# Optimization experiments

Measured on AMD Instinct MI355X. Metric: run time of the kernel, lower is better.

The kernel has to match this reference:

```python
import jax, jax.numpy as jnp
import numpy as np

H = 50  # hidden_size

def setup_inputs() -> dict:
    key = jax.random.key(0)
    ks = jax.random.split(key, 7)
    B, T, I = 8192, 2048, 1
    s_ih = 1.0 / np.sqrt(H)
    x = jax.random.normal(ks[0], (B, T, I), dtype=jnp.float32)
    # PyTorch nn.LSTM params, gate order (i, f, g, o)
    W_ih = jax.random.uniform(ks[1], (4 * H, I), minval=-s_ih, maxval=s_ih, dtype=jnp.float32)
    W_hh = jax.random.uniform(ks[2], (4 * H, H), minval=-s_ih, maxval=s_ih, dtype=jnp.float32)
    b_ih = jax.random.uniform(ks[3], (4 * H,), minval=-s_ih, maxval=s_ih, dtype=jnp.float32)
    b_hh = jax.random.uniform(ks[4], (4 * H,), minval=-s_ih, maxval=s_ih, dtype=jnp.float32)
    W_lin = jax.random.uniform(ks[5], (1, H), minval=-s_ih, maxval=s_ih, dtype=jnp.float32)
    b_lin = jax.random.uniform(ks[6], (1,), minval=-s_ih, maxval=s_ih, dtype=jnp.float32)
    return {"x": x, "W_ih": W_ih, "W_hh": W_hh, "b_ih": b_ih, "b_hh": b_hh,
            "W_lin": W_lin, "b_lin": b_lin}

def _lstm_last_h(x, W_ih, W_hh, b_ih, b_hh):
    B = x.shape[0]
    # precompute input contribution per timestep: [T, B, 4H]
    xg = jnp.einsum('bti,gi->tbg', x, W_ih) + (b_ih + b_hh)  # [T,B,4H]

    def step(carry, xg_t):
        h, c = carry
        z = xg_t + h @ W_hh.T  # [B,4H]
        i = jax.nn.sigmoid(z[:, :H])
        f = jax.nn.sigmoid(z[:, H:2 * H])
        g = jnp.tanh(z[:, 2 * H:3 * H])
        o = jax.nn.sigmoid(z[:, 3 * H:])
        c = f * c + i * g
        h = o * jnp.tanh(c)
        return (h, c), None

    h0 = jnp.zeros((B, H), dtype=x.dtype)
    c0 = jnp.zeros((B, H), dtype=x.dtype)
    (h_last, _), _ = jax.lax.scan(step, (h0, c0), xg)
    return h_last  # [B,H]

def reference(x, W_ih, W_hh, b_ih, b_hh, W_lin, b_lin):
    h_last = _lstm_last_h(x, W_ih, W_hh, b_ih, b_hh)
    return h_last @ W_lin.T + b_lin  # [B,1]
```

## Files before the change

kernel.cpp:

```cpp
#include <hip/hip_runtime.h>


#define HID   50
#define NSTEP 2048
#define BPB   16
#define HSTR  72

typedef _Float16 half8   __attribute__((ext_vector_type(8)));
typedef float    float4v __attribute__((ext_vector_type(4)));
typedef float    float2v __attribute__((ext_vector_type(2)));

__device__ __forceinline__ float2v lo2(float4v v) { float2v r; r[0] = v[0]; r[1] = v[1]; return r; }
__device__ __forceinline__ float2v hi2(float4v v) { float2v r; r[0] = v[2]; r[1] = v[3]; return r; }

__device__ __forceinline__ float2v exp2v(float2v x) {
    float2v r;
    r[0] = __builtin_amdgcn_exp2f(x[0]);
    r[1] = __builtin_amdgcn_exp2f(x[1]);
    return r;
}

__device__ __forceinline__ float2v gate_pairs2(float2v zi, float2v zf, float2v zg,
                                               float2v zo, float2v& c) {
    float2v ei = exp2v(zi);
    float2v ef = exp2v(zf);
    float2v Eg = exp2v(zg);
    float2v eo = exp2v(zo);
    float2v t1  = (1.0f + ei) * (1.0f + Eg);
    float2v pf  = 1.0f + ef;
    float2v num = c * t1 + pf * (Eg - 1.0f);
    float2v D   = t1 * pf;
    float   rP  = __builtin_amdgcn_rcpf(D[0] * D[1]);
    float2v Dsw; Dsw[0] = D[1]; Dsw[1] = D[0];
    c = num * Dsw * rP;
    float2v a = 2.8853900817779268f * c;
    a[0] = fminf(fmaxf(a[0], -24.0f), 24.0f);
    a[1] = fminf(fmaxf(a[1], -24.0f), 24.0f);
    float2v Ec  = exp2v(a);
    float2v den = (1.0f + eo) * (1.0f + Ec);
    float   rQ  = __builtin_amdgcn_rcpf(den[0] * den[1]);
    float2v dsw; dsw[0] = den[1]; dsw[1] = den[0];
    return (Ec - 1.0f) * dsw * rQ;
}

__global__ __launch_bounds__(256, 2) void lstm_fused(
    const float* __restrict__ x,
    const float* __restrict__ W_ih,
    const float* __restrict__ W_hh,
    const float* __restrict__ b_ih,
    const float* __restrict__ b_hh,
    const float* __restrict__ W_lin,
    const float* __restrict__ b_lin,
    float* __restrict__ out)
{
    __shared__ __align__(16) _Float16 hbuf[2][BPB][HSTR];

    const int tid  = threadIdx.x;
    const int wave = tid >> 6;
    const int lane = tid & 63;
    const int col  = lane & 15;
    const int quad = lane >> 4;
    const int b0   = blockIdx.x * BPB;
    const int j    = wave * 16 + col;

    for (int i = tid; i < 2 * BPB * HSTR; i += 256)
        (&hbuf[0][0][0])[i] = (_Float16)0.0f;
    __syncthreads();
    if (tid < BPB) {
        hbuf[0][tid][HID]     = (_Float16)x[(size_t)(b0 + tid) * NSTEP];
        hbuf[0][tid][HID + 1] = (_Float16)1.0f;
        hbuf[1][tid][HID + 1] = (_Float16)1.0f;
    }

    const float LOG2E = 1.4426950408889634f;
    half8 bfrag[4][2];
    for (int g = 0; g < 4; ++g) {
        const float sc = (g == 2) ? (2.0f * LOG2E) : (-LOG2E);
        for (int kt = 0; kt < 2; ++kt) {
            half8 f;
            #pragma unroll
            for (int jj = 0; jj < 8; ++jj) {
                int k = kt * 32 + quad * 8 + jj;
                float v = 0.0f;
                if (j < HID) {
                    int row = g * HID + j;
                    if (k < HID)           v = W_hh[row * HID + k];
                    else if (k == HID)     v = W_ih[row];
                    else if (k == HID + 1) v = b_ih[row] + b_hh[row];
                }
                f[jj] = (_Float16)(v * sc);
            }
            bfrag[g][kt] = f;
        }
    }

    float2v c01 = {0.f, 0.f};
    float2v c23 = {0.f, 0.f};
    const bool xloader = (wave == 3) && (quad == 0);
    const float* xrow = x + (size_t)(b0 + col) * NSTEP;
    const float4v Z4 = {0.f, 0.f, 0.f, 0.f};

    __syncthreads();

    if (blockIdx.x & 1) {
        __builtin_amdgcn_s_sleep(15);
    }

#define STEP(CUR, NXT, T)                                                        \
    {                                                                            \
        float xn = 0.f;                                                          \
        if (xloader) {                                                           \
            int tt = ((T) + 1 < NSTEP) ? ((T) + 1) : (NSTEP - 1);                \
            xn = xrow[tt];                                                       \
        }                                                                        \
        const _Float16* arow = &hbuf[CUR][col][0];                               \
        half8 a0 = *(const half8*)(arow + quad * 8);                             \
        half8 a1 = *(const half8*)(arow + 32 + quad * 8);                        \
        float4v d0, d1, d2, d3;                                                  \
        d0 = __builtin_amdgcn_mfma_f32_16x16x32_f16(a0, bfrag[0][0], Z4, 0, 0, 0); \
        d1 = __builtin_amdgcn_mfma_f32_16x16x32_f16(a0, bfrag[1][0], Z4, 0, 0, 0); \
        d2 = __builtin_amdgcn_mfma_f32_16x16x32_f16(a0, bfrag[2][0], Z4, 0, 0, 0); \
        d3 = __builtin_amdgcn_mfma_f32_16x16x32_f16(a0, bfrag[3][0], Z4, 0, 0, 0); \
        d0 = __builtin_amdgcn_mfma_f32_16x16x32_f16(a1, bfrag[0][1], d0, 0, 0, 0); \
        d1 = __builtin_amdgcn_mfma_f32_16x16x32_f16(a1, bfrag[1][1], d1, 0, 0, 0); \
        d2 = __builtin_amdgcn_mfma_f32_16x16x32_f16(a1, bfrag[2][1], d2, 0, 0, 0); \
        d3 = __builtin_amdgcn_mfma_f32_16x16x32_f16(a1, bfrag[3][1], d3, 0, 0, 0); \
        float2v h01 = gate_pairs2(lo2(d0), lo2(d1), lo2(d2), lo2(d3), c01);      \
        if (j < HID) {                                                           \
            hbuf[NXT][quad * 4 + 0][j] = (_Float16)h01[0];                       \
            hbuf[NXT][quad * 4 + 1][j] = (_Float16)h01[1];                       \
        }                                                                        \
        float2v h23 = gate_pairs2(hi2(d0), hi2(d1), hi2(d2), hi2(d3), c23);      \
        if (j < HID) {                                                           \
            hbuf[NXT][quad * 4 + 2][j] = (_Float16)h23[0];                       \
            hbuf[NXT][quad * 4 + 3][j] = (_Float16)h23[1];                       \
        }                                                                        \
        if (xloader)                                                             \
            hbuf[NXT][col][HID] = (_Float16)xn;                                  \
        __syncthreads();                                                         \
    }

    for (int t = 0; t < NSTEP; t += 2) {
        STEP(0, 1, t)
        STEP(1, 0, t + 1)
    }
#undef STEP

    if (tid < BPB) {
        float s = b_lin[0];
        for (int k = 0; k < HID; ++k)
            s += (float)hbuf[0][tid][k] * W_lin[k];
        out[b0 + tid] = s;
    }
}

extern "C" void kernel_launch(void* const* d_in, const int* in_sizes, int n_in,
                              void* d_out, int out_size, void* d_ws, size_t ws_size,
                              hipStream_t stream) {
    const float* x     = (const float*)d_in[0];
    const float* W_ih  = (const float*)d_in[1];
    const float* W_hh  = (const float*)d_in[2];
    const float* b_ih  = (const float*)d_in[3];
    const float* b_hh  = (const float*)d_in[4];
    const float* W_lin = (const float*)d_in[5];
    const float* b_lin = (const float*)d_in[6];
    float* outp = (float*)d_out;
    dim3 grid(8192 / BPB), block(256);
    hipLaunchKernelGGL(lstm_fused, grid, block, 0, stream,
                       x, W_ih, W_hh, b_ih, b_hh, W_lin, b_lin, outp);
}
```

Baseline: 1.338 ms.

## Process two 16-row batch tiles per block to interleave independent recurrences

```diff
diff --git a/kernel.cpp b/kernel.cpp
--- a/kernel.cpp
+++ b/kernel.cpp
@@ -3,7 +3,7 @@
 
 #define HID   50
 #define NSTEP 2048
-#define BPB   16
+#define BPB   32
 #define HSTR  72
 
 typedef _Float16 half8   __attribute__((ext_vector_type(8)));
@@ -43,7 +43,7 @@
     return (Ec - 1.0f) * dsw * rQ;
 }
 
-__global__ __launch_bounds__(256, 2) void lstm_fused(
+__global__ __launch_bounds__(256, 1) void lstm_fused(
     const float* __restrict__ x,
     const float* __restrict__ W_ih,
     const float* __restrict__ W_hh,
@@ -53,7 +53,7 @@
     const float* __restrict__ b_lin,
     float* __restrict__ out)
 {
-    __shared__ __align__(16) _Float16 hbuf[2][BPB][HSTR];
+    __shared__ __align__(16) _Float16 hbuf[2][2][16][HSTR];
 
     const int tid  = threadIdx.x;
     const int wave = tid >> 6;
@@ -63,13 +63,14 @@
     const int b0   = blockIdx.x * BPB;
     const int j    = wave * 16 + col;
 
-    for (int i = tid; i < 2 * BPB * HSTR; i += 256)
-        (&hbuf[0][0][0])[i] = (_Float16)0.0f;
+    for (int i = tid; i < 2 * 2 * 16 * HSTR; i += 256)
+        (&hbuf[0][0][0][0])[i] = (_Float16)0.0f;
     __syncthreads();
     if (tid < BPB) {
-        hbuf[0][tid][HID]     = (_Float16)x[(size_t)(b0 + tid) * NSTEP];
-        hbuf[0][tid][HID + 1] = (_Float16)1.0f;
-        hbuf[1][tid][HID + 1] = (_Float16)1.0f;
+        int g = tid >> 4, r = tid & 15;
+        hbuf[0][g][r][HID]     = (_Float16)x[(size_t)(b0 + tid) * NSTEP];
+        hbuf[0][g][r][HID + 1] = (_Float16)1.0f;
+        hbuf[1][g][r][HID + 1] = (_Float16)1.0f;
     }
 
     const float LOG2E = 1.4426950408889634f;
@@ -94,50 +95,62 @@
         }
     }
 
-    float2v c01 = {0.f, 0.f};
-    float2v c23 = {0.f, 0.f};
-    const bool xloader = (wave == 3) && (quad == 0);
-    const float* xrow = x + (size_t)(b0 + col) * NSTEP;
+    float2v cA01 = {0.f, 0.f}, cA23 = {0.f, 0.f};
+    float2v cB01 = {0.f, 0.f}, cB23 = {0.f, 0.f};
+
+    const bool xloader = (wave == 3) && (quad < 2);
+    const float* xrow = x + (size_t)(b0 + quad * 16 + col) * NSTEP;
     const float4v Z4 = {0.f, 0.f, 0.f, 0.f};
 
     __syncthreads();
 
-    if (blockIdx.x & 1) {
-        __builtin_amdgcn_s_sleep(15);
-    }
-
-#define STEP(CUR, NXT, T)                                                        \
-    {                                                                            \
-        float xn = 0.f;                                                          \
-        if (xloader) {                                                           \
-            int tt = ((T) + 1 < NSTEP) ? ((T) + 1) : (NSTEP - 1);                \
-            xn = xrow[tt];                                                       \
-        }                                                                        \
-        const _Float16* arow = &hbuf[CUR][col][0];                               \
-        half8 a0 = *(const half8*)(arow + quad * 8);                             \
-        half8 a1 = *(const half8*)(arow + 32 + quad * 8);                        \
-        float4v d0, d1, d2, d3;                                                  \
-        d0 = __builtin_amdgcn_mfma_f32_16x16x32_f16(a0, bfrag[0][0], Z4, 0, 0, 0); \
-        d1 = __builtin_amdgcn_mfma_f32_16x16x32_f16(a0, bfrag[1][0], Z4, 0, 0, 0); \
-        d2 = __builtin_amdgcn_mfma_f32_16x16x32_f16(a0, bfrag[2][0], Z4, 0, 0, 0); \
-        d3 = __builtin_amdgcn_mfma_f32_16x16x32_f16(a0, bfrag[3][0], Z4, 0, 0, 0); \
-        d0 = __builtin_amdgcn_mfma_f32_16x16x32_f16(a1, bfrag[0][1], d0, 0, 0, 0); \
-        d1 = __builtin_amdgcn_mfma_f32_16x16x32_f16(a1, bfrag[1][1], d1, 0, 0, 0); \
-        d2 = __builtin_amdgcn_mfma_f32_16x16x32_f16(a1, bfrag[2][1], d2, 0, 0, 0); \
-        d3 = __builtin_amdgcn_mfma_f32_16x16x32_f16(a1, bfrag[3][1], d3, 0, 0, 0); \
-        float2v h01 = gate_pairs2(lo2(d0), lo2(d1), lo2(d2), lo2(d3), c01);      \
-        if (j < HID) {                                                           \
-            hbuf[NXT][quad * 4 + 0][j] = (_Float16)h01[0];                       \
-            hbuf[NXT][quad * 4 + 1][j] = (_Float16)h01[1];                       \
-        }                                                                        \
-        float2v h23 = gate_pairs2(hi2(d0), hi2(d1), hi2(d2), hi2(d3), c23);      \
-        if (j < HID) {                                                           \
-            hbuf[NXT][quad * 4 + 2][j] = (_Float16)h23[0];                       \
-            hbuf[NXT][quad * 4 + 3][j] = (_Float16)h23[1];                       \
-        }                                                                        \
-        if (xloader)                                                             \
-            hbuf[NXT][col][HID] = (_Float16)xn;                                  \
-        __syncthreads();                                                         \
+#define STEP(CUR, NXT, T)                                                          \
+    {                                                                              \
+        float xn = 0.f;                                                            \
+        if (xloader) {                                                             \
+            int tt = ((T) + 1 < NSTEP) ? ((T) + 1) : (NSTEP - 1);                  \
+            xn = xrow[tt];                                                         \
+        }                                                                          \
+        const _Float16* arowA = &hbuf[CUR][0][col][0];                             \
+        const _Float16* arowB = &hbuf[CUR][1][col][0];                             \
+        half8 A0 = *(const half8*)(arowA + quad * 8);                              \
+        half8 A1 = *(const half8*)(arowA + 32 + quad * 8);                         \
+        half8 B0 = *(const half8*)(arowB + quad * 8);                              \
+        half8 B1 = *(const half8*)(arowB + 32 + quad * 8);                         \
+        float4v dA0, dA1, dA2, dA3, dB0, dB1, dB2, dB3;                            \
+        dA0 = __builtin_amdgcn_mfma_f32_16x16x32_f16(A0, bfrag[0][0], Z4, 0, 0, 0); \
+        dA1 = __builtin_amdgcn_mfma_f32_16x16x32_f16(A0, bfrag[1][0], Z4, 0, 0, 0); \
+        dA2 = __builtin_amdgcn_mfma_f32_16x16x32_f16(A0, bfrag[2][0], Z4, 0, 0, 0); \
+        dA3 = __builtin_amdgcn_mfma_f32_16x16x32_f16(A0, bfrag[3][0], Z4, 0, 0, 0); \
+        dB0 = __builtin_amdgcn_mfma_f32_16x16x32_f16(B0, bfrag[0][0], Z4, 0, 0, 0); \
+        dB1 = __builtin_amdgcn_mfma_f32_16x16x32_f16(B0, bfrag[1][0], Z4, 0, 0, 0); \
+        dB2 = __builtin_amdgcn_mfma_f32_16x16x32_f16(B0, bfrag[2][0], Z4, 0, 0, 0); \
+        dB3 = __builtin_amdgcn_mfma_f32_16x16x32_f16(B0, bfrag[3][0], Z4, 0, 0, 0); \
+        dA0 = __builtin_amdgcn_mfma_f32_16x16x32_f16(A1, bfrag[0][1], dA0, 0, 0, 0); \
+        dA1 = __builtin_amdgcn_mfma_f32_16x16x32_f16(A1, bfrag[1][1], dA1, 0, 0, 0); \
+        dA2 = __builtin_amdgcn_mfma_f32_16x16x32_f16(A1, bfrag[2][1], dA2, 0, 0, 0); \
+        dA3 = __builtin_amdgcn_mfma_f32_16x16x32_f16(A1, bfrag[3][1], dA3, 0, 0, 0); \
+        dB0 = __builtin_amdgcn_mfma_f32_16x16x32_f16(B1, bfrag[0][1], dB0, 0, 0, 0); \
+        dB1 = __builtin_amdgcn_mfma_f32_16x16x32_f16(B1, bfrag[1][1], dB1, 0, 0, 0); \
+        dB2 = __builtin_amdgcn_mfma_f32_16x16x32_f16(B1, bfrag[2][1], dB2, 0, 0, 0); \
+        dB3 = __builtin_amdgcn_mfma_f32_16x16x32_f16(B1, bfrag[3][1], dB3, 0, 0, 0); \
+        float2v hA01 = gate_pairs2(lo2(dA0), lo2(dA1), lo2(dA2), lo2(dA3), cA01);  \
+        float2v hB01 = gate_pairs2(lo2(dB0), lo2(dB1), lo2(dB2), lo2(dB3), cB01);  \
+        float2v hA23 = gate_pairs2(hi2(dA0), hi2(dA1), hi2(dA2), hi2(dA3), cA23);  \
+        float2v hB23 = gate_pairs2(hi2(dB0), hi2(dB1), hi2(dB2), hi2(dB3), cB23);  \
+        if (j < HID) {                                                             \
+            hbuf[NXT][0][quad * 4 + 0][j] = (_Float16)hA01[0];                     \
+            hbuf[NXT][0][quad * 4 + 1][j] = (_Float16)hA01[1];                     \
+            hbuf[NXT][0][quad * 4 + 2][j] = (_Float16)hA23[0];                     \
+            hbuf[NXT][0][quad * 4 + 3][j] = (_Float16)hA23[1];                     \
+            hbuf[NXT][1][quad * 4 + 0][j] = (_Float16)hB01[0];                     \
+            hbuf[NXT][1][quad * 4 + 1][j] = (_Float16)hB01[1];                     \
+            hbuf[NXT][1][quad * 4 + 2][j] = (_Float16)hB23[0];                     \
+            hbuf[NXT][1][quad * 4 + 3][j] = (_Float16)hB23[1];                     \
+        }                                                                          \
+        if (xloader)                                                               \
+            hbuf[NXT][quad][col][HID] = (_Float16)xn;                              \
+        __syncthreads();                                                           \
     }
 
     for (int t = 0; t < NSTEP; t += 2) {
@@ -147,9 +160,10 @@
 #undef STEP
 
     if (tid < BPB) {
+        int g = tid >> 4, r = tid & 15;
         float s = b_lin[0];
         for (int k = 0; k < HID; ++k)
-            s += (float)hbuf[0][tid][k] * W_lin[k];
+            s += (float)hbuf[0][g][r][k] * W_lin[k];
         out[b0 + tid] = s;
     }
 }
```

New measurement: 1.543 ms. 15.4% more time.

## Interleave two 16-sequence groups per block to overlap MFMA with gate math

Applied to the files above, without the earlier changes.

```diff
diff --git a/kernel.cpp b/kernel.cpp
--- a/kernel.cpp
+++ b/kernel.cpp
@@ -3,7 +3,7 @@
 
 #define HID   50
 #define NSTEP 2048
-#define BPB   16
+#define BPB   32
 #define HSTR  72
 
 typedef _Float16 half8   __attribute__((ext_vector_type(8)));
@@ -43,7 +43,7 @@
     return (Ec - 1.0f) * dsw * rQ;
 }
 
-__global__ __launch_bounds__(256, 2) void lstm_fused(
+__global__ __launch_bounds__(256, 1) void lstm_fused(
     const float* __restrict__ x,
     const float* __restrict__ W_ih,
     const float* __restrict__ W_hh,
@@ -53,7 +53,7 @@
     const float* __restrict__ b_lin,
     float* __restrict__ out)
 {
-    __shared__ __align__(16) _Float16 hbuf[2][BPB][HSTR];
+    __shared__ __align__(16) _Float16 hbuf[2][16][HSTR];
 
     const int tid  = threadIdx.x;
     const int wave = tid >> 6;
@@ -63,13 +63,13 @@
     const int b0   = blockIdx.x * BPB;
     const int j    = wave * 16 + col;
 
-    for (int i = tid; i < 2 * BPB * HSTR; i += 256)
+    for (int i = tid; i < 2 * 16 * HSTR; i += 256)
         (&hbuf[0][0][0])[i] = (_Float16)0.0f;
     __syncthreads();
     if (tid < BPB) {
-        hbuf[0][tid][HID]     = (_Float16)x[(size_t)(b0 + tid) * NSTEP];
-        hbuf[0][tid][HID + 1] = (_Float16)1.0f;
-        hbuf[1][tid][HID + 1] = (_Float16)1.0f;
+        int g = tid >> 4, r = tid & 15;
+        hbuf[g][r][HID]     = (_Float16)x[(size_t)(b0 + tid) * NSTEP];
+        hbuf[g][r][HID + 1] = (_Float16)1.0f;
     }
 
     const float LOG2E = 1.4426950408889634f;
@@ -94,62 +94,99 @@
         }
     }
 
-    float2v c01 = {0.f, 0.f};
-    float2v c23 = {0.f, 0.f};
+    float2v cA01 = {0.f, 0.f}, cA23 = {0.f, 0.f};
+    float2v cB01 = {0.f, 0.f}, cB23 = {0.f, 0.f};
+
     const bool xloader = (wave == 3) && (quad == 0);
-    const float* xrow = x + (size_t)(b0 + col) * NSTEP;
+    const float* xrowA = x + (size_t)(b0 + col) * NSTEP;
+    const float* xrowB = x + (size_t)(b0 + 16 + col) * NSTEP;
     const float4v Z4 = {0.f, 0.f, 0.f, 0.f};
 
     __syncthreads();
 
-    if (blockIdx.x & 1) {
-        __builtin_amdgcn_s_sleep(15);
-    }
-
-#define STEP(CUR, NXT, T)                                                        \
-    {                                                                            \
-        float xn = 0.f;                                                          \
-        if (xloader) {                                                           \
-            int tt = ((T) + 1 < NSTEP) ? ((T) + 1) : (NSTEP - 1);                \
-            xn = xrow[tt];                                                       \
-        }                                                                        \
-        const _Float16* arow = &hbuf[CUR][col][0];                               \
-        half8 a0 = *(const half8*)(arow + quad * 8);                             \
-        half8 a1 = *(const half8*)(arow + 32 + quad * 8);                        \
-        float4v d0, d1, d2, d3;                                                  \
-        d0 = __builtin_amdgcn_mfma_f32_16x16x32_f16(a0, bfrag[0][0], Z4, 0, 0, 0); \
-        d1 = __builtin_amdgcn_mfma_f32_16x16x32_f16(a0, bfrag[1][0], Z4, 0, 0, 0); \
-        d2 = __builtin_amdgcn_mfma_f32_16x16x32_f16(a0, bfrag[2][0], Z4, 0, 0, 0); \
-        d3 = __builtin_amdgcn_mfma_f32_16x16x32_f16(a0, bfrag[3][0], Z4, 0, 0, 0); \
-        d0 = __builtin_amdgcn_mfma_f32_16x16x32_f16(a1, bfrag[0][1], d0, 0, 0, 0); \
-        d1 = __builtin_amdgcn_mfma_f32_16x16x32_f16(a1, bfrag[1][1], d1, 0, 0, 0); \
-        d2 = __builtin_amdgcn_mfma_f32_16x16x32_f16(a1, bfrag[2][1], d2, 0, 0, 0); \
-        d3 = __builtin_amdgcn_mfma_f32_16x16x32_f16(a1, bfrag[3][1], d3, 0, 0, 0); \
-        float2v h01 = gate_pairs2(lo2(d0), lo2(d1), lo2(d2), lo2(d3), c01);      \
-        if (j < HID) {                                                           \
-            hbuf[NXT][quad * 4 + 0][j] = (_Float16)h01[0];                       \
-            hbuf[NXT][quad * 4 + 1][j] = (_Float16)h01[1];                       \
-        }                                                                        \
-        float2v h23 = gate_pairs2(hi2(d0), hi2(d1), hi2(d2), hi2(d3), c23);      \
-        if (j < HID) {                                                           \
-            hbuf[NXT][quad * 4 + 2][j] = (_Float16)h23[0];                       \
-            hbuf[NXT][quad * 4 + 3][j] = (_Float16)h23[1];                       \
-        }                                                                        \
-        if (xloader)                                                             \
-            hbuf[NXT][col][HID] = (_Float16)xn;                                  \
-        __syncthreads();                                                         \
-    }
-
-    for (int t = 0; t < NSTEP; t += 2) {
-        STEP(0, 1, t)
-        STEP(1, 0, t + 1)
-    }
-#undef STEP
+    float4v zA0, zA1, zA2, zA3, zB0, zB1, zB2, zB3;
+
+    {
+        const _Float16* ar = &hbuf[1][col][0];
+        half8 a0 = *(const half8*)(ar + quad * 8);
+        half8 a1 = *(const half8*)(ar + 32 + quad * 8);
+        zB0 = __builtin_amdgcn_mfma_f32_16x16x32_f16(a0, bfrag[0][0], Z4, 0, 0, 0);
+        zB1 = __builtin_amdgcn_mfma_f32_16x16x32_f16(a0, bfrag[1][0], Z4, 0, 0, 0);
+        zB2 = __builtin_amdgcn_mfma_f32_16x16x32_f16(a0, bfrag[2][0], Z4, 0, 0, 0);
+        zB3 = __builtin_amdgcn_mfma_f32_16x16x32_f16(a0, bfrag[3][0], Z4, 0, 0, 0);
+        zB0 = __builtin_amdgcn_mfma_f32_16x16x32_f16(a1, bfrag[0][1], zB0, 0, 0, 0);
+        zB1 = __builtin_amdgcn_mfma_f32_16x16x32_f16(a1, bfrag[1][1], zB1, 0, 0, 0);
+        zB2 = __builtin_amdgcn_mfma_f32_16x16x32_f16(a1, bfrag[2][1], zB2, 0, 0, 0);
+        zB3 = __builtin_amdgcn_mfma_f32_16x16x32_f16(a1, bfrag[3][1], zB3, 0, 0, 0);
+    }
+    __syncthreads();
+
+    for (int t = 0; t < NSTEP; ++t) {
+        {
+            float xn = 0.f;
+            if (xloader) {
+                int tt = (t + 1 < NSTEP) ? (t + 1) : (NSTEP - 1);
+                xn = xrowB[tt];
+            }
+            const _Float16* ar = &hbuf[0][col][0];
+            half8 a0 = *(const half8*)(ar + quad * 8);
+            half8 a1 = *(const half8*)(ar + 32 + quad * 8);
+            float2v h01 = gate_pairs2(lo2(zB0), lo2(zB1), lo2(zB2), lo2(zB3), cB01);
+            float2v h23 = gate_pairs2(hi2(zB0), hi2(zB1), hi2(zB2), hi2(zB3), cB23);
+            zA0 = __builtin_amdgcn_mfma_f32_16x16x32_f16(a0, bfrag[0][0], Z4, 0, 0, 0);
+            zA1 = __builtin_amdgcn_mfma_f32_16x16x32_f16(a0, bfrag[1][0], Z4, 0, 0, 0);
+            zA2 = __builtin_amdgcn_mfma_f32_16x16x32_f16(a0, bfrag[2][0], Z4, 0, 0, 0);
+            zA3 = __builtin_amdgcn_mfma_f32_16x16x32_f16(a0, bfrag[3][0], Z4, 0, 0, 0);
+            zA0 = __builtin_amdgcn_mfma_f32_16x16x32_f16(a1, bfrag[0][1], zA0, 0, 0, 0);
+            zA1 = __builtin_amdgcn_mfma_f32_16x16x32_f16(a1, bfrag[1][1], zA1, 0, 0, 0);
+            zA2 = __builtin_amdgcn_mfma_f32_16x16x32_f16(a1, bfrag[2][1], zA2, 0, 0, 0);
+            zA3 = __builtin_amdgcn_mfma_f32_16x16x32_f16(a1, bfrag[3][1], zA3, 0, 0, 0);
+            if (j < HID) {
+                hbuf[1][quad * 4 + 0][j] = (_Float16)h01[0];
+                hbuf[1][quad * 4 + 1][j] = (_Float16)h01[1];
+                hbuf[1][quad * 4 + 2][j] = (_Float16)h23[0];
+                hbuf[1][quad * 4 + 3][j] = (_Float16)h23[1];
+            }
+            if (xloader)
+                hbuf[1][col][HID] = (_Float16)xn;
+            __syncthreads();
+        }
+        {
+            float xn = 0.f;
+            if (xloader) {
+                int tt = (t + 1 < NSTEP) ? (t + 1) : (NSTEP - 1);
+                xn = xrowA[tt];
+            }
+            const _Float16* ar = &hbuf[1][col][0];
+            half8 a0 = *(const half8*)(ar + quad * 8);
+            half8 a1 = *(const half8*)(ar + 32 + quad * 8);
+            float2v h01 = gate_pairs2(lo2(zA0), lo2(zA1), lo2(zA2), lo2(zA3), cA01);
+            float2v h23 = gate_pairs2(hi2(zA0), hi2(zA1), hi2(zA2), hi2(zA3), cA23);
+            zB0 = __builtin_amdgcn_mfma_f32_16x16x32_f16(a0, bfrag[0][0], Z4, 0, 0, 0);
+            zB1 = __builtin_amdgcn_mfma_f32_16x16x32_f16(a0, bfrag[1][0], Z4, 0, 0, 0);
+            zB2 = __builtin_amdgcn_mfma_f32_16x16x32_f16(a0, bfrag[2][0], Z4, 0, 0, 0);
+            zB3 = __builtin_amdgcn_mfma_f32_16x16x32_f16(a0, bfrag[3][0], Z4, 0, 0, 0);
+            zB0 = __builtin_amdgcn_mfma_f32_16x16x32_f16(a1, bfrag[0][1], zB0, 0, 0, 0);
+            zB1 = __builtin_amdgcn_mfma_f32_16x16x32_f16(a1, bfrag[1][1], zB1, 0, 0, 0);
+            zB2 = __builtin_amdgcn_mfma_f32_16x16x32_f16(a1, bfrag[2][1], zB2, 0, 0, 0);
+            zB3 = __builtin_amdgcn_mfma_f32_16x16x32_f16(a1, bfrag[3][1], zB3, 0, 0, 0);
+            if (j < HID) {
+                hbuf[0][quad * 4 + 0][j] = (_Float16)h01[0];
+                hbuf[0][quad * 4 + 1][j] = (_Float16)h01[1];
+                hbuf[0][quad * 4 + 2][j] = (_Float16)h23[0];
+                hbuf[0][quad * 4 + 3][j] = (_Float16)h23[1];
+            }
+            if (xloader)
+                hbuf[0][col][HID] = (_Float16)xn;
+            __syncthreads();
+        }
+    }
 
     if (tid < BPB) {
+        int g = tid >> 4, r = tid & 15;
         float s = b_lin[0];
         for (int k = 0; k < HID; ++k)
-            s += (float)hbuf[0][tid][k] * W_lin[k];
+            s += (float)hbuf[g][r][k] * W_lin[k];
         out[b0 + tid] = s;
     }
 }
```

After: 1.947 ms. +45.6%, slower.
